# Kernel optimization log

Measured on AMD Instinct MI355X. Metric: run time of the kernel, lower is better.

## Reference

```python
import jax, jax.numpy as jnp
import numpy as np
import math

STRIDE = 32
CTR_CLAMP = 32.0
SCALE_CLAMP = math.log(1000.0 / 16)  # DEFAULT_SCALE_CLAMP
CONF_THRESH = 0.05
NMS_THRESH = 0.6
TOPK = 1000
NUM_CLASSES = 80
CLASS_OFFSET = 1.0e5  # separates classes so one IoU pass == per-class NMS


def setup_inputs() -> dict:
    key = jax.random.key(0)
    k1, k2 = jax.random.split(key)
    fmp_h, fmp_w = 100, 100
    A = 5
    M = fmp_h * fmp_w * A  # 50000 candidates
    cls_pred = jax.random.normal(k1, (M, NUM_CLASSES), dtype=jnp.float32)
    reg_pred = jax.random.normal(k2, (M, 4), dtype=jnp.float32)
    anchor_size = jnp.array([[32, 32], [64, 64], [128, 128], [256, 256], [512, 512]], dtype=jnp.float32)
    return {"cls_pred": cls_pred, "reg_pred": reg_pred, "anchor_size": anchor_size,
            "fmp_h": fmp_h, "fmp_w": fmp_w}


def _generate_anchors(anchor_size, fmp_h, fmp_w):
    # anchors laid out as [H*W, A, 4] -> [M, 4], matching torch.meshgrid order
    ys, xs = jnp.meshgrid(jnp.arange(fmp_h, dtype=jnp.float32),
                          jnp.arange(fmp_w, dtype=jnp.float32), indexing="ij")
    xy = (jnp.stack([xs, ys], axis=-1).reshape(-1, 2) + 0.5) * STRIDE  # [HW, 2]
    A = anchor_size.shape[0]
    anchor_xy = jnp.repeat(xy[:, None, :], A, axis=1)                   # [HW, A, 2]
    anchor_wh = jnp.broadcast_to(anchor_size[None], (xy.shape[0], A, 2))
    return jnp.concatenate([anchor_xy, anchor_wh], axis=-1).reshape(-1, 4)  # [M, 4]


def _decode_boxes(anchors, reg):
    # anchors/reg: [K, 4] (cx, cy, w, h) / (dx, dy, dw, dh)
    ctr_off = jnp.clip(reg[:, :2] * anchors[:, 2:], -CTR_CLAMP, CTR_CLAMP)
    ctr_xy = anchors[:, :2] + ctr_off
    wh = anchors[:, 2:] * jnp.exp(jnp.minimum(reg[:, 2:], SCALE_CLAMP))
    return jnp.concatenate([ctr_xy - 0.5 * wh, ctr_xy + 0.5 * wh], axis=-1)  # x1y1x2y2


def _greedy_nms_keep(boxes, valid):
    # boxes: [K, 4] already score-sorted descending; valid: [K] bool
    x1, y1, x2, y2 = boxes[:, 0], boxes[:, 1], boxes[:, 2], boxes[:, 3]
    areas = (x2 - x1) * (y2 - y1)
    xx1 = jnp.maximum(x1[:, None], x1[None, :])
    yy1 = jnp.maximum(y1[:, None], y1[None, :])
    xx2 = jnp.minimum(x2[:, None], x2[None, :])
    yy2 = jnp.minimum(y2[:, None], y2[None, :])
    inter = jnp.maximum(1e-28, xx2 - xx1) * jnp.maximum(1e-28, yy2 - yy1)
    iou = inter / (areas[:, None] + areas[None, :] - inter + 1e-14)  # [K, K]
    idxs = jnp.arange(boxes.shape[0])

    def body(i, keep):
        suppress = keep[i] & (iou[i] > NMS_THRESH) & (idxs > i)
        return keep & ~suppress

    return jax.lax.fori_loop(0, boxes.shape[0], body, valid)


def reference(cls_pred, reg_pred, anchor_size, fmp_h, fmp_w):
    anchors = _generate_anchors(anchor_size, fmp_h, fmp_w)  # [M, 4]
    probs = jax.nn.sigmoid(cls_pred)                        # [M, C]
    scores = probs.max(axis=-1)
    labels = probs.argmax(axis=-1)
    # top-k candidates (lax.top_k returns scores sorted descending)
    scores, idx = jax.lax.top_k(scores, TOPK)
    labels = labels[idx]
    reg = reg_pred[idx]
    anc = anchors[idx]
    boxes = _decode_boxes(anc, reg)                         # [K, 4] in pixels
    valid = scores >= CONF_THRESH
    # per-class NMS via class offsets (boxes of different classes never overlap)
    boxes_off = boxes + labels.astype(boxes.dtype)[:, None] * CLASS_OFFSET
    keep = _greedy_nms_keep(boxes_off, valid)
    img_w = fmp_w * STRIDE
    img_h = fmp_h * STRIDE
    scale = jnp.array([img_w, img_h, img_w, img_h], dtype=boxes.dtype)
    nboxes = jnp.clip(boxes / scale, 0.0, 1.0)
    m = keep.astype(boxes.dtype)
    return nboxes * m[:, None], scores * m, jnp.where(keep, labels, -1), keep
```

## Files before the change

### kernel.cpp

```cpp
#include <hip/hip_runtime.h>
#include <math.h>

#define NCLS 80
#define TOPK 1000
#define NWORDS 16
#define CAND_CAP 4096

__device__ __forceinline__ float sigmoid_np(float x) {
  float e = (float)exp(-(double)x);
  return 1.0f / (1.0f + e);
}
__device__ __forceinline__ float exp_np(float x) { return (float)exp((double)x); }

__device__ __forceinline__ unsigned fkey(float s) {
  unsigned u = __float_as_uint(s);
  return ((int)u < 0) ? ~u : (u | 0x80000000u);
}

__device__ __forceinline__ void agg_add(unsigned* h, unsigned bin, bool pred) {
  unsigned long long rem = __ballot(pred);
  const int lane = threadIdx.x & 63;
  while (rem) {
    int leader = __ffsll(rem) - 1;
    unsigned lb = (unsigned)__shfl((int)bin, leader, 64);
    unsigned long long m = __ballot(pred && bin == lb);
    if (lane == leader) atomicAdd(&h[lb], (unsigned)__popcll(m));
    rem &= ~m;
  }
}

__launch_bounds__(1024)
__global__ void k_score(const float* __restrict__ cls, float* __restrict__ scores,
                        int* __restrict__ labels, unsigned* __restrict__ ghist1, int M) {
  __shared__ unsigned h1[4096];
  const int t = threadIdx.x;
  #pragma unroll
  for (int k = 0; k < 4; ++k) h1[t + 1024 * k] = 0u;
  __syncthreads();

  int gid = blockIdx.x * 1024 + t;
  int anchor = gid >> 2;
  int q = gid & 3;
  bool act = anchor < M;
  float lv[20];
  float best = -3.4e38f; int bc = 0;
  if (act) {
    const float4* row = reinterpret_cast<const float4*>(cls) + (size_t)anchor * (NCLS / 4);
    #pragma unroll
    for (int k = 0; k < 5; ++k) {
      float4 v = row[q + 4 * k];
      int cbase = (q + 4 * k) * 4;
      lv[4 * k + 0] = v.x; lv[4 * k + 1] = v.y; lv[4 * k + 2] = v.z; lv[4 * k + 3] = v.w;
      if (v.x > best) { best = v.x; bc = cbase + 0; }
      if (v.y > best) { best = v.y; bc = cbase + 1; }
      if (v.z > best) { best = v.z; bc = cbase + 2; }
      if (v.w > best) { best = v.w; bc = cbase + 3; }
    }
  } else {
    #pragma unroll
    for (int k = 0; k < 20; ++k) lv[k] = -3.4e38f;
  }
  #pragma unroll
  for (int d = 1; d < 4; d <<= 1) {
    float ob = __shfl_xor(best, d, 64);
    int oc = __shfl_xor(bc, d, 64);
    if (ob > best || (ob == best && oc < bc)) { best = ob; bc = oc; }
  }
  float s = sigmoid_np(best);
  float sp = s * (1.0f - s);
  float band = (s < 1.0f && sp > 0.0f) ? (4.8e-7f / sp) : 3.4e38f;
  float thresh = best - band;
  int cclose = 1 << 30;
  #pragma unroll
  for (int k = 0; k < 5; ++k) {
    #pragma unroll
    for (int j = 0; j < 4; ++j) {
      int c = (q + 4 * k) * 4 + j;
      if (lv[4 * k + j] >= thresh && c < cclose) cclose = c;
    }
  }
  #pragma unroll
  for (int d = 1; d < 4; d <<= 1) {
    int oc = __shfl_xor(cclose, d, 64);
    if (oc < cclose) cclose = oc;
  }
  int lab = bc;
  if (act && cclose < bc && q == 0) {
    float bp = -1.0f; int bl = 0;
    for (int c = 0; c < NCLS; ++c) {
      float p = sigmoid_np(cls[(size_t)anchor * NCLS + c]);
      if (p > bp) { bp = p; bl = c; }
    }
    lab = bl;
  }
  if (act && q == 0) {
    scores[anchor] = s;
    labels[anchor] = lab;
  }
  agg_add(h1, fkey(s) >> 20, act && q == 0);
  __syncthreads();
  #pragma unroll
  for (int k = 0; k < 4; ++k) {
    unsigned c = h1[t + 1024 * k];
    if (c) atomicAdd(&ghist1[t + 1024 * k], c);
  }
}

__launch_bounds__(1024)
__global__ void k_hist2(const unsigned* __restrict__ ghist1, const float* __restrict__ scores,
                        unsigned* __restrict__ ghist2, unsigned* __restrict__ gmeta, int M) {
  __shared__ unsigned chunks[1024];
  __shared__ int sB1; __shared__ unsigned sAb;
  const int t = threadIdx.x;
  unsigned hb0 = ghist1[4 * t], hb1 = ghist1[4 * t + 1],
           hb2 = ghist1[4 * t + 2], hb3 = ghist1[4 * t + 3];
  chunks[t] = hb0 + hb1 + hb2 + hb3;
  __syncthreads();
  for (int d = 1; d < 1024; d <<= 1) {
    unsigned v = chunks[t] + ((t + d < 1024) ? chunks[t + d] : 0u);
    __syncthreads();
    chunks[t] = v;
    __syncthreads();
  }
  {
    unsigned ssc = chunks[t];
    unsigned ssn = (t + 1 < 1024) ? chunks[t + 1] : 0u;
    if (ssc >= (unsigned)TOPK && ssn < (unsigned)TOPK) {
      unsigned hb[4] = {hb0, hb1, hb2, hb3};
      unsigned run = ssn;
      for (int b = 3; b >= 0; --b) {
        run += hb[b];
        if (run >= (unsigned)TOPK) { sB1 = 4 * t + b; sAb = run - hb[b]; break; }
      }
    }
  }
  __syncthreads();
  const unsigned B1 = (unsigned)sB1;
  if (blockIdx.x == 0 && t == 0) { gmeta[0] = B1; gmeta[1] = sAb; }

  int base = (blockIdx.x * 1024 + t) * 4;
  if (base + 3 < M) {
    float4 v = *reinterpret_cast<const float4*>(scores + base);
    unsigned k0 = fkey(v.x), k1 = fkey(v.y), k2 = fkey(v.z), k3 = fkey(v.w);
    if ((k0 >> 20) == B1) atomicAdd(&ghist2[(k0 >> 8) & 0xFFFu], 1u);
    if ((k1 >> 20) == B1) atomicAdd(&ghist2[(k1 >> 8) & 0xFFFu], 1u);
    if ((k2 >> 20) == B1) atomicAdd(&ghist2[(k2 >> 8) & 0xFFFu], 1u);
    if ((k3 >> 20) == B1) atomicAdd(&ghist2[(k3 >> 8) & 0xFFFu], 1u);
  } else {
    for (int j = base; j < M; ++j) {
      unsigned k0 = fkey(scores[j]);
      if ((k0 >> 20) == B1) atomicAdd(&ghist2[(k0 >> 8) & 0xFFFu], 1u);
    }
  }
}

__launch_bounds__(1024)
__global__ void k_compact(const unsigned* __restrict__ ghist2, const unsigned* __restrict__ gmeta,
                          const float* __restrict__ scores,
                          unsigned long long* __restrict__ cand, unsigned* __restrict__ gcount,
                          int M) {
  __shared__ unsigned chunks[1024];
  __shared__ int sB2;
  __shared__ unsigned wcnt[16];
  __shared__ unsigned sbase;
  const int t = threadIdx.x;
  const unsigned B1 = gmeta[0], nAb = gmeta[1];
  unsigned hb0 = ghist2[4 * t], hb1 = ghist2[4 * t + 1],
           hb2 = ghist2[4 * t + 2], hb3 = ghist2[4 * t + 3];
  chunks[t] = hb0 + hb1 + hb2 + hb3;
  __syncthreads();
  for (int d = 1; d < 1024; d <<= 1) {
    unsigned v = chunks[t] + ((t + d < 1024) ? chunks[t + d] : 0u);
    __syncthreads();
    chunks[t] = v;
    __syncthreads();
  }
  {
    unsigned ssc = nAb + chunks[t];
    unsigned ssn = nAb + ((t + 1 < 1024) ? chunks[t + 1] : 0u);
    if (ssc >= (unsigned)TOPK && ssn < (unsigned)TOPK) {
      unsigned hb[4] = {hb0, hb1, hb2, hb3};
      unsigned run = ssn;
      for (int b = 3; b >= 0; --b) {
        run += hb[b];
        if (run >= (unsigned)TOPK) { sB2 = 4 * t + b; break; }
      }
    }
  }
  __syncthreads();
  const unsigned T = (B1 << 20) | ((unsigned)sB2 << 8);

  int base = (blockIdx.x * 1024 + t) * 4;
  unsigned keys[4]; int idxs[4]; int np = 0;
  #pragma unroll
  for (int j = 0; j < 4; ++j) {
    int i = base + j;
    if (i < M) {
      unsigned key = fkey(scores[i]);
      if (key >= T) { keys[np] = key; idxs[np] = i; ++np; }
    }
  }
  const int lane = t & 63, wid = t >> 6;
  int sc = np;
  #pragma unroll
  for (int d = 1; d < 64; d <<= 1) {
    int o = __shfl_up(sc, d, 64);
    if (lane >= d) sc += o;
  }
  if (lane == 63) wcnt[wid] = (unsigned)sc;
  __syncthreads();
  if (t == 0) {
    unsigned acc = 0;
    for (int w = 0; w < 16; ++w) { unsigned v = wcnt[w]; wcnt[w] = acc; acc += v; }
    sbase = acc ? atomicAdd(gcount, acc) : 0u;
  }
  __syncthreads();
  unsigned pos = sbase + wcnt[wid] + (unsigned)(sc - np);
  for (int j = 0; j < np; ++j) {
    if (pos < (unsigned)CAND_CAP)
      cand[pos] = ((unsigned long long)keys[j] << 32) | (unsigned)(~(unsigned)idxs[j]);
    ++pos;
  }
}

__launch_bounds__(1024)
__global__ void k_rank(const unsigned long long* __restrict__ cand, const unsigned* __restrict__ gcount,
                       const int* __restrict__ labels, const float* __restrict__ reg,
                       const float* __restrict__ asz, const int* __restrict__ pW, int A,
                       float* __restrict__ sel_score, int* __restrict__ sel_label,
                       float* __restrict__ boxes, float* __restrict__ areas,
                       float* __restrict__ obox) {
  __shared__ unsigned long long ck[CAND_CAP];
  const int t = threadIdx.x;
  unsigned n = *gcount; if (n > (unsigned)CAND_CAP) n = (unsigned)CAND_CAP;
  for (int i = t; i < CAND_CAP; i += 1024) ck[i] = (i < (int)n) ? cand[i] : 0ull;
  __syncthreads();
  for (int c = t; c < (int)n; c += 1024) {
    unsigned long long my = ck[c];
    int r = 0;
    for (int j = 0; j < (int)n; ++j) r += (ck[j] > my);
    if (r < TOPK) {
      unsigned key = (unsigned)(my >> 32);
      unsigned u = (key & 0x80000000u) ? (key ^ 0x80000000u) : ~key;
      float scv = __uint_as_float(u);
      int idx = (int)(~(unsigned)my);
      int lab = labels[idx];
      int W = *pW;
      int a = idx % A;
      int cell = idx / A;
      int x = cell % W;
      int y = cell / W;
      float aw = asz[a * 2 + 0], ah = asz[a * 2 + 1];
      float ax = ((float)x + 0.5f) * 32.0f;
      float ay = ((float)y + 0.5f) * 32.0f;
      float4 rg = *reinterpret_cast<const float4*>(reg + (size_t)idx * 4);
      float offx = fminf(fmaxf(rg.x * aw, -32.0f), 32.0f);
      float offy = fminf(fmaxf(rg.y * ah, -32.0f), 32.0f);
      float cx = ax + offx, cy = ay + offy;
      const float SC = 4.135166556742356f;
      float bw = aw * exp_np(fminf(rg.z, SC));
      float bh = ah * exp_np(fminf(rg.w, SC));
      float x1 = cx - 0.5f * bw, y1 = cy - 0.5f * bh;
      float x2 = cx + 0.5f * bw, y2 = cy + 0.5f * bh;
      float off = (float)lab * 100000.0f;
      float ox1 = x1 + off, oy1 = y1 + off, ox2 = x2 + off, oy2 = y2 + off;
      sel_score[r] = scv; sel_label[r] = lab;
      boxes[r * 4 + 0] = x1; boxes[r * 4 + 1] = y1;
      boxes[r * 4 + 2] = x2; boxes[r * 4 + 3] = y2;
      obox[0 * 1024 + r] = ox1; obox[1 * 1024 + r] = oy1;
      obox[2 * 1024 + r] = ox2; obox[3 * 1024 + r] = oy2;
      areas[r] = (ox2 - ox1) * (oy2 - oy1);
    }
  }
}

__launch_bounds__(256)
__global__ void k_mask(const float* __restrict__ obox, const float* __restrict__ areas,
                       unsigned long long* __restrict__ maskC) {
  __shared__ float so0[1024], so1[1024], so2[1024], so3[1024], sa[1024];
  const int t = threadIdx.x;
  int g = blockIdx.x * 256 + t;
  int c = g >> 10, j = g & 1023;
  for (int idx = t; idx < 1024; idx += 256) {
    so0[idx] = obox[idx];        so1[idx] = obox[1024 + idx];
    so2[idx] = obox[2048 + idx]; so3[idx] = obox[3072 + idx];
    sa[idx] = areas[idx];
  }
  __syncthreads();
  if (j >= TOPK) { maskC[c * 1024 + j] = 0ull; return; }
  float x1j = so0[j], y1j = so1[j], x2j = so2[j], y2j = so3[j];
  float aj = sa[j];
  unsigned long long bits = 0ull;
  int i0 = c * 64;
  for (int ii = 0; ii < 64; ++ii) {
    int i = i0 + ii;
    if (i < TOPK && i < j) {
      float xx1 = fmaxf(so0[i], x1j);
      float yy1 = fmaxf(so1[i], y1j);
      float xx2 = fminf(so2[i], x2j);
      float yy2 = fminf(so3[i], y2j);
      float inter = fmaxf(1e-28f, xx2 - xx1) * fmaxf(1e-28f, yy2 - yy1);
      float uni = sa[i] + aj - inter + 1e-14f;
      float iou = inter / uni;
      if (iou > 0.6f) bits |= (1ull << ii);
    }
  }
  maskC[c * 1024 + j] = bits;
}

__launch_bounds__(512, 1)
__global__ void k_nms(const unsigned long long* __restrict__ maskC,
                      const float* __restrict__ sel_score, const int* __restrict__ sel_label,
                      const float* __restrict__ boxes,
                      const int* __restrict__ pW, const int* __restrict__ pH,
                      float* __restrict__ out) {
  __shared__ unsigned long long sm[16 * 16 * 64];
  __shared__ float ssc[1024];
  __shared__ unsigned long long kwS[16];
  const int tid = threadIdx.x;
  const int wv = tid >> 6, lane = tid & 63;

  {
    int pair = 0;
    #pragma unroll
    for (int f = 0; f < 16; ++f) {
      #pragma unroll
      for (int g = f; g < 16; ++g) {
        if ((pair & 7) == wv)
          sm[(f * 16 + g) * 64 + lane] = maskC[f * 1024 + g * 64 + lane];
        ++pair;
      }
    }
  }
  for (int i = tid; i < 1024; i += 512)
    ssc[i] = (i < TOPK) ? sel_score[i] : 0.0f;
  __syncthreads();

  if (tid < 64) {
    unsigned long long supp[16];
    #pragma unroll
    for (int f = 0; f < 16; ++f) supp[f] = 0ull;
    #pragma unroll
    for (int f = 0; f < 16; ++f) {
      unsigned long long ct = sm[(f * 16 + f) * 64 + lane];
      unsigned long long w[16];
      #pragma unroll
      for (int g = f + 1; g < 16; ++g) w[g] = sm[(f * 16 + g) * 64 + lane];
      int r = f * 64 + lane;
      unsigned long long valid = __ballot((r < TOPK) && (ssc[r] >= 0.05f));
      unsigned long long sup_any = __ballot(ct != 0ull);
      unsigned long long avail = valid & ~supp[f];
      unsigned long long kwf = 0ull;
      while (avail) {
        unsigned long long fs = avail & sup_any;
        if (!fs) { kwf |= avail; break; }
        int i = __ffsll((long long)fs) - 1;
        unsigned long long below = (1ull << i) - 1ull;
        kwf |= avail & below;
        kwf |= (1ull << i);
        unsigned long long vict = __ballot(((ct >> i) & 1ull) != 0ull);
        avail &= ~vict;
        avail &= ~(below | (1ull << i));
      }
      if (lane == 0) kwS[f] = kwf;
      #pragma unroll
      for (int g = f + 1; g < 16; ++g)
        supp[g] |= __ballot((w[g] & kwf) != 0ull);
    }
  }
  __syncthreads();

  float sw = (float)(*pW * 32);
  float sh = (float)(*pH * 32);
  const float4* b4 = reinterpret_cast<const float4*>(boxes);
  for (int r = tid; r < TOPK; r += 512) {
    bool kp = (kwS[r >> 6] >> (r & 63)) & 1ull;
    float m = kp ? 1.0f : 0.0f;
    float4 b = b4[r];
    float b0 = fminf(fmaxf(b.x / sw, 0.0f), 1.0f) * m;
    float b1 = fminf(fmaxf(b.y / sh, 0.0f), 1.0f) * m;
    float b2 = fminf(fmaxf(b.z / sw, 0.0f), 1.0f) * m;
    float b3 = fminf(fmaxf(b.w / sh, 0.0f), 1.0f) * m;
    out[r * 4 + 0] = b0; out[r * 4 + 1] = b1;
    out[r * 4 + 2] = b2; out[r * 4 + 3] = b3;
    out[TOPK * 4 + r] = ssc[r] * m;
    out[TOPK * 5 + r] = kp ? (float)sel_label[r] : -1.0f;
    out[TOPK * 6 + r] = m;
  }
}

extern "C" void kernel_launch(void* const* d_in, const int* in_sizes, int n_in,
                              void* d_out, int out_size, void* d_ws, size_t ws_size,
                              hipStream_t stream) {
  const float* cls = (const float*)d_in[0];
  const float* reg = (const float*)d_in[1];
  const float* asz = (const float*)d_in[2];
  const int* pH = (const int*)d_in[3];
  const int* pW = (const int*)d_in[4];
  int M = in_sizes[0] / NCLS;
  int A = in_sizes[2] / 2;

  char* ws = (char*)d_ws;
  size_t off = 0;
  auto alloc = [&](size_t bytes) { size_t o = off; off = (off + bytes + 255) & ~(size_t)255; return o; };
  size_t o_h1    = alloc(4096 * sizeof(unsigned));
  size_t o_h2    = alloc(4096 * sizeof(unsigned));
  size_t o_misc  = alloc(256);
  size_t zero_end = off;
  size_t o_cand  = alloc((size_t)CAND_CAP * sizeof(unsigned long long));
  size_t o_sc    = alloc((size_t)M * sizeof(float));
  size_t o_lb    = alloc((size_t)M * sizeof(int));
  size_t o_ssc   = alloc(1024 * sizeof(float));
  size_t o_slb   = alloc(1024 * sizeof(int));
  size_t o_box   = alloc((size_t)TOPK * 4 * sizeof(float));
  size_t o_area  = alloc(1024 * sizeof(float));
  size_t o_obox  = alloc(4 * 1024 * sizeof(float));
  size_t o_mask  = alloc((size_t)NWORDS * 1024 * sizeof(unsigned long long));
  (void)ws_size; (void)out_size; (void)n_in;

  hipMemsetAsync(ws, 0, zero_end, stream);

  int nblk_score = (M * 4 + 1023) / 1024;
  k_score<<<nblk_score, 1024, 0, stream>>>(
      cls, (float*)(ws + o_sc), (int*)(ws + o_lb), (unsigned*)(ws + o_h1), M);

  int nblk_scan = ((M + 3) / 4 + 1023) / 1024;
  k_hist2<<<nblk_scan, 1024, 0, stream>>>(
      (const unsigned*)(ws + o_h1), (const float*)(ws + o_sc),
      (unsigned*)(ws + o_h2), (unsigned*)(ws + o_misc + 8), M);
  k_compact<<<nblk_scan, 1024, 0, stream>>>(
      (const unsigned*)(ws + o_h2), (const unsigned*)(ws + o_misc + 8),
      (const float*)(ws + o_sc),
      (unsigned long long*)(ws + o_cand), (unsigned*)(ws + o_misc), M);
  k_rank<<<1, 1024, 0, stream>>>(
      (const unsigned long long*)(ws + o_cand), (const unsigned*)(ws + o_misc),
      (const int*)(ws + o_lb), reg, asz, pW, A,
      (float*)(ws + o_ssc), (int*)(ws + o_slb),
      (float*)(ws + o_box), (float*)(ws + o_area), (float*)(ws + o_obox));
  k_mask<<<(NWORDS * 1024) / 256, 256, 0, stream>>>(
      (const float*)(ws + o_obox), (const float*)(ws + o_area),
      (unsigned long long*)(ws + o_mask));
  k_nms<<<1, 512, 0, stream>>>(
      (const unsigned long long*)(ws + o_mask),
      (const float*)(ws + o_ssc), (const int*)(ws + o_slb),
      (const float*)(ws + o_box), pW, pH, (float*)d_out);
}
```

Measured before the change: 76.77 us.

## Fuse all pipeline stages into one cooperative persistent kernel with grid syncs

Replaces the memset and six separate kernel launches with a single cooperative kernel of 256 blocks by 512 threads. Stages are separated by grid.sync instead of kernel boundaries, and shared memory is reused through a union. The NMS mask tiles are also stored compactly in upper-triangular form. The aim is to remove per-launch overhead and the idle gaps between small serial stages, in exchange for grid-wide barrier cost and lower parallelism in the wide scoring stage.

```diff
diff --git a/kernel.cpp b/kernel.cpp
--- a/kernel.cpp
+++ b/kernel.cpp
@@ -1,10 +1,15 @@
 #include <hip/hip_runtime.h>
+#include <hip/hip_cooperative_groups.h>
 #include <math.h>
+
+namespace cg = cooperative_groups;
 
 #define NCLS 80
 #define TOPK 1000
-#define NWORDS 16
 #define CAND_CAP 4096
+#define NBLK 256
+#define NTHR 512
+#define TRI_IDX(f, g) ((f) * 16 - ((f) * ((f) - 1)) / 2 + ((g) - (f)))
 
 __device__ __forceinline__ float sigmoid_np(float x) {
   float e = (float)exp(-(double)x);
@@ -29,363 +34,340 @@
   }
 }
 
-__launch_bounds__(1024)
-__global__ void k_score(const float* __restrict__ cls, float* __restrict__ scores,
-                        int* __restrict__ labels, unsigned* __restrict__ ghist1, int M) {
-  __shared__ unsigned h1[4096];
-  const int t = threadIdx.x;
+union BigLds {
+  unsigned h1[4096];
+  unsigned chunks[512];
+  unsigned long long ck[CAND_CAP];
+  struct { float so0[1024], so1[1024], so2[1024], so3[1024], sa[1024]; } d;
+  struct { unsigned long long sm[8704]; float ssc[1024];
+           int pf[136], pg[136]; unsigned long long kwS[16]; } e;
+};
+
+__global__ void __launch_bounds__(512) k_all(
+    const float* __restrict__ cls, const float* __restrict__ reg,
+    const float* __restrict__ asz, const int* __restrict__ pW,
+    const int* __restrict__ pH,
+    float* __restrict__ scores, int* __restrict__ labels,
+    unsigned* __restrict__ ghist1, unsigned* __restrict__ ghist2,
+    unsigned* __restrict__ gcount, unsigned long long* __restrict__ cand,
+    float* __restrict__ sel_score, int* __restrict__ sel_label,
+    float* __restrict__ boxesO, float* __restrict__ areas,
+    float* __restrict__ obox, unsigned long long* __restrict__ maskC,
+    float* __restrict__ out, int M, int A) {
+  cg::grid_group grid = cg::this_grid();
+  const int tid = threadIdx.x;
+  const int b = blockIdx.x;
+  const int tg = b * NTHR + tid;
+  const int lane = tid & 63;
+  __shared__ BigLds L;
+  __shared__ int sB1; __shared__ unsigned sAb; __shared__ int sB2;
+
+  if (tg < 4096) ghist1[tg] = 0u;
+  else if (tg < 8192) ghist2[tg - 4096] = 0u;
+  else if (tg == 8192) *gcount = 0u;
+  grid.sync();
+
   #pragma unroll
-  for (int k = 0; k < 4; ++k) h1[t + 1024 * k] = 0u;
-  __syncthreads();
-
-  int gid = blockIdx.x * 1024 + t;
-  int anchor = gid >> 2;
-  int q = gid & 3;
-  bool act = anchor < M;
-  float lv[20];
-  float best = -3.4e38f; int bc = 0;
-  if (act) {
-    const float4* row = reinterpret_cast<const float4*>(cls) + (size_t)anchor * (NCLS / 4);
-    #pragma unroll
-    for (int k = 0; k < 5; ++k) {
-      float4 v = row[q + 4 * k];
-      int cbase = (q + 4 * k) * 4;
-      lv[4 * k + 0] = v.x; lv[4 * k + 1] = v.y; lv[4 * k + 2] = v.z; lv[4 * k + 3] = v.w;
-      if (v.x > best) { best = v.x; bc = cbase + 0; }
-      if (v.y > best) { best = v.y; bc = cbase + 1; }
-      if (v.z > best) { best = v.z; bc = cbase + 2; }
-      if (v.w > best) { best = v.w; bc = cbase + 3; }
-    }
-  } else {
-    #pragma unroll
-    for (int k = 0; k < 20; ++k) lv[k] = -3.4e38f;
-  }
-  #pragma unroll
-  for (int d = 1; d < 4; d <<= 1) {
-    float ob = __shfl_xor(best, d, 64);
-    int oc = __shfl_xor(bc, d, 64);
-    if (ob > best || (ob == best && oc < bc)) { best = ob; bc = oc; }
-  }
-  float s = sigmoid_np(best);
-  float sp = s * (1.0f - s);
-  float band = (s < 1.0f && sp > 0.0f) ? (4.8e-7f / sp) : 3.4e38f;
-  float thresh = best - band;
-  int cclose = 1 << 30;
-  #pragma unroll
-  for (int k = 0; k < 5; ++k) {
-    #pragma unroll
-    for (int j = 0; j < 4; ++j) {
-      int c = (q + 4 * k) * 4 + j;
-      if (lv[4 * k + j] >= thresh && c < cclose) cclose = c;
-    }
-  }
-  #pragma unroll
-  for (int d = 1; d < 4; d <<= 1) {
-    int oc = __shfl_xor(cclose, d, 64);
-    if (oc < cclose) cclose = oc;
-  }
-  int lab = bc;
-  if (act && cclose < bc && q == 0) {
-    float bp = -1.0f; int bl = 0;
-    for (int c = 0; c < NCLS; ++c) {
-      float p = sigmoid_np(cls[(size_t)anchor * NCLS + c]);
-      if (p > bp) { bp = p; bl = c; }
-    }
-    lab = bl;
-  }
-  if (act && q == 0) {
-    scores[anchor] = s;
-    labels[anchor] = lab;
-  }
-  agg_add(h1, fkey(s) >> 20, act && q == 0);
+  for (int k = 0; k < 8; ++k) L.h1[tid + 512 * k] = 0u;
   __syncthreads();
   #pragma unroll
-  for (int k = 0; k < 4; ++k) {
-    unsigned c = h1[t + 1024 * k];
-    if (c) atomicAdd(&ghist1[t + 1024 * k], c);
-  }
-}
-
-__launch_bounds__(1024)
-__global__ void k_hist2(const unsigned* __restrict__ ghist1, const float* __restrict__ scores,
-                        unsigned* __restrict__ ghist2, unsigned* __restrict__ gmeta, int M) {
-  __shared__ unsigned chunks[1024];
-  __shared__ int sB1; __shared__ unsigned sAb;
-  const int t = threadIdx.x;
-  unsigned hb0 = ghist1[4 * t], hb1 = ghist1[4 * t + 1],
-           hb2 = ghist1[4 * t + 2], hb3 = ghist1[4 * t + 3];
-  chunks[t] = hb0 + hb1 + hb2 + hb3;
+  for (int k = 0; k < 2; ++k) {
+    int task = tg + k * (NBLK * NTHR);
+    int anchor = task >> 2, q = task & 3;
+    bool act = anchor < M;
+    float lv[20];
+    float best = -3.4e38f; int bc = 0;
+    if (act) {
+      const float4* row = reinterpret_cast<const float4*>(cls) + (size_t)anchor * (NCLS / 4);
+      #pragma unroll
+      for (int kk = 0; kk < 5; ++kk) {
+        float4 v = row[q + 4 * kk];
+        int cbase = (q + 4 * kk) * 4;
+        lv[4 * kk + 0] = v.x; lv[4 * kk + 1] = v.y; lv[4 * kk + 2] = v.z; lv[4 * kk + 3] = v.w;
+        if (v.x > best) { best = v.x; bc = cbase + 0; }
+        if (v.y > best) { best = v.y; bc = cbase + 1; }
+        if (v.z > best) { best = v.z; bc = cbase + 2; }
+        if (v.w > best) { best = v.w; bc = cbase + 3; }
+      }
+    } else {
+      #pragma unroll
+      for (int kk = 0; kk < 20; ++kk) lv[kk] = -3.4e38f;
+    }
+    #pragma unroll
+    for (int d = 1; d < 4; d <<= 1) {
+      float ob = __shfl_xor(best, d, 64);
+      int oc = __shfl_xor(bc, d, 64);
+      if (ob > best || (ob == best && oc < bc)) { best = ob; bc = oc; }
+    }
+    float s = sigmoid_np(best);
+    float sp = s * (1.0f - s);
+    float band = (s < 1.0f && sp > 0.0f) ? (4.8e-7f / sp) : 3.4e38f;
+    float thresh = best - band;
+    int cclose = 1 << 30;
+    #pragma unroll
+    for (int kk = 0; kk < 5; ++kk) {
+      #pragma unroll
+      for (int j = 0; j < 4; ++j) {
+        int c = (q + 4 * kk) * 4 + j;
+        if (lv[4 * kk + j] >= thresh && c < cclose) cclose = c;
+      }
+    }
+    #pragma unroll
+    for (int d = 1; d < 4; d <<= 1) {
+      int oc = __shfl_xor(cclose, d, 64);
+      if (oc < cclose) cclose = oc;
+    }
+    int lab = bc;
+    if (act && cclose < bc && q == 0) {
+      float bp = -1.0f; int bl = 0;
+      for (int c = 0; c < NCLS; ++c) {
+        float p = sigmoid_np(cls[(size_t)anchor * NCLS + c]);
+        if (p > bp) { bp = p; bl = c; }
+      }
+      lab = bl;
+    }
+    if (act && q == 0) { scores[anchor] = s; labels[anchor] = lab; }
+    agg_add(L.h1, fkey(s) >> 20, act && q == 0);
+  }
   __syncthreads();
-  for (int d = 1; d < 1024; d <<= 1) {
-    unsigned v = chunks[t] + ((t + d < 1024) ? chunks[t + d] : 0u);
-    __syncthreads();
-    chunks[t] = v;
-    __syncthreads();
-  }
+  #pragma unroll
+  for (int k = 0; k < 8; ++k) {
+    unsigned c = L.h1[tid + 512 * k];
+    if (c) atomicAdd(&ghist1[tid + 512 * k], c);
+  }
+  grid.sync();
+
   {
-    unsigned ssc = chunks[t];
-    unsigned ssn = (t + 1 < 1024) ? chunks[t + 1] : 0u;
+    unsigned hb[8];
+    #pragma unroll
+    for (int i = 0; i < 8; ++i) hb[i] = ghist1[tid * 8 + i];
+    unsigned s8 = hb[0] + hb[1] + hb[2] + hb[3] + hb[4] + hb[5] + hb[6] + hb[7];
+    L.chunks[tid] = s8;
+    __syncthreads();
+    for (int d = 1; d < 512; d <<= 1) {
+      unsigned v = L.chunks[tid] + ((tid + d < 512) ? L.chunks[tid + d] : 0u);
+      __syncthreads(); L.chunks[tid] = v; __syncthreads();
+    }
+    unsigned ssc = L.chunks[tid];
+    unsigned ssn = (tid + 1 < 512) ? L.chunks[tid + 1] : 0u;
     if (ssc >= (unsigned)TOPK && ssn < (unsigned)TOPK) {
-      unsigned hb[4] = {hb0, hb1, hb2, hb3};
       unsigned run = ssn;
-      for (int b = 3; b >= 0; --b) {
-        run += hb[b];
-        if (run >= (unsigned)TOPK) { sB1 = 4 * t + b; sAb = run - hb[b]; break; }
-      }
-    }
-  }
-  __syncthreads();
+      for (int bb = 7; bb >= 0; --bb) {
+        run += hb[bb];
+        if (run >= (unsigned)TOPK) { sB1 = tid * 8 + bb; sAb = run - hb[bb]; break; }
+      }
+    }
+    __syncthreads();
+  }
   const unsigned B1 = (unsigned)sB1;
-  if (blockIdx.x == 0 && t == 0) { gmeta[0] = B1; gmeta[1] = sAb; }
-
-  int base = (blockIdx.x * 1024 + t) * 4;
-  if (base + 3 < M) {
-    float4 v = *reinterpret_cast<const float4*>(scores + base);
+  const unsigned nAb = sAb;
+  const int M4 = M >> 2;
+  const float4* s4 = reinterpret_cast<const float4*>(scores);
+  if (tg < M4) {
+    float4 v = s4[tg];
     unsigned k0 = fkey(v.x), k1 = fkey(v.y), k2 = fkey(v.z), k3 = fkey(v.w);
     if ((k0 >> 20) == B1) atomicAdd(&ghist2[(k0 >> 8) & 0xFFFu], 1u);
     if ((k1 >> 20) == B1) atomicAdd(&ghist2[(k1 >> 8) & 0xFFFu], 1u);
     if ((k2 >> 20) == B1) atomicAdd(&ghist2[(k2 >> 8) & 0xFFFu], 1u);
     if ((k3 >> 20) == B1) atomicAdd(&ghist2[(k3 >> 8) & 0xFFFu], 1u);
-  } else {
-    for (int j = base; j < M; ++j) {
-      unsigned k0 = fkey(scores[j]);
-      if ((k0 >> 20) == B1) atomicAdd(&ghist2[(k0 >> 8) & 0xFFFu], 1u);
-    }
-  }
-}
-
-__launch_bounds__(1024)
-__global__ void k_compact(const unsigned* __restrict__ ghist2, const unsigned* __restrict__ gmeta,
-                          const float* __restrict__ scores,
-                          unsigned long long* __restrict__ cand, unsigned* __restrict__ gcount,
-                          int M) {
-  __shared__ unsigned chunks[1024];
-  __shared__ int sB2;
-  __shared__ unsigned wcnt[16];
-  __shared__ unsigned sbase;
-  const int t = threadIdx.x;
-  const unsigned B1 = gmeta[0], nAb = gmeta[1];
-  unsigned hb0 = ghist2[4 * t], hb1 = ghist2[4 * t + 1],
-           hb2 = ghist2[4 * t + 2], hb3 = ghist2[4 * t + 3];
-  chunks[t] = hb0 + hb1 + hb2 + hb3;
-  __syncthreads();
-  for (int d = 1; d < 1024; d <<= 1) {
-    unsigned v = chunks[t] + ((t + d < 1024) ? chunks[t + d] : 0u);
-    __syncthreads();
-    chunks[t] = v;
-    __syncthreads();
-  }
+  }
+  grid.sync();
+
   {
-    unsigned ssc = nAb + chunks[t];
-    unsigned ssn = nAb + ((t + 1 < 1024) ? chunks[t + 1] : 0u);
+    unsigned hb[8];
+    #pragma unroll
+    for (int i = 0; i < 8; ++i) hb[i] = ghist2[tid * 8 + i];
+    unsigned s8 = hb[0] + hb[1] + hb[2] + hb[3] + hb[4] + hb[5] + hb[6] + hb[7];
+    L.chunks[tid] = s8;
+    __syncthreads();
+    for (int d = 1; d < 512; d <<= 1) {
+      unsigned v = L.chunks[tid] + ((tid + d < 512) ? L.chunks[tid + d] : 0u);
+      __syncthreads(); L.chunks[tid] = v; __syncthreads();
+    }
+    unsigned ssc = nAb + L.chunks[tid];
+    unsigned ssn = nAb + ((tid + 1 < 512) ? L.chunks[tid + 1] : 0u);
     if (ssc >= (unsigned)TOPK && ssn < (unsigned)TOPK) {
-      unsigned hb[4] = {hb0, hb1, hb2, hb3};
       unsigned run = ssn;
-      for (int b = 3; b >= 0; --b) {
-        run += hb[b];
-        if (run >= (unsigned)TOPK) { sB2 = 4 * t + b; break; }
-      }
-    }
-  }
-  __syncthreads();
+      for (int bb = 7; bb >= 0; --bb) {
+        run += hb[bb];
+        if (run >= (unsigned)TOPK) { sB2 = tid * 8 + bb; break; }
+      }
+    }
+    __syncthreads();
+  }
   const unsigned T = (B1 << 20) | ((unsigned)sB2 << 8);
-
-  int base = (blockIdx.x * 1024 + t) * 4;
-  unsigned keys[4]; int idxs[4]; int np = 0;
-  #pragma unroll
-  for (int j = 0; j < 4; ++j) {
-    int i = base + j;
-    if (i < M) {
-      unsigned key = fkey(scores[i]);
-      if (key >= T) { keys[np] = key; idxs[np] = i; ++np; }
-    }
-  }
-  const int lane = t & 63, wid = t >> 6;
-  int sc = np;
-  #pragma unroll
-  for (int d = 1; d < 64; d <<= 1) {
-    int o = __shfl_up(sc, d, 64);
-    if (lane >= d) sc += o;
-  }
-  if (lane == 63) wcnt[wid] = (unsigned)sc;
-  __syncthreads();
-  if (t == 0) {
-    unsigned acc = 0;
-    for (int w = 0; w < 16; ++w) { unsigned v = wcnt[w]; wcnt[w] = acc; acc += v; }
-    sbase = acc ? atomicAdd(gcount, acc) : 0u;
-  }
-  __syncthreads();
-  unsigned pos = sbase + wcnt[wid] + (unsigned)(sc - np);
-  for (int j = 0; j < np; ++j) {
-    if (pos < (unsigned)CAND_CAP)
-      cand[pos] = ((unsigned long long)keys[j] << 32) | (unsigned)(~(unsigned)idxs[j]);
-    ++pos;
-  }
-}
-
-__launch_bounds__(1024)
-__global__ void k_rank(const unsigned long long* __restrict__ cand, const unsigned* __restrict__ gcount,
-                       const int* __restrict__ labels, const float* __restrict__ reg,
-                       const float* __restrict__ asz, const int* __restrict__ pW, int A,
-                       float* __restrict__ sel_score, int* __restrict__ sel_label,
-                       float* __restrict__ boxes, float* __restrict__ areas,
-                       float* __restrict__ obox) {
-  __shared__ unsigned long long ck[CAND_CAP];
-  const int t = threadIdx.x;
-  unsigned n = *gcount; if (n > (unsigned)CAND_CAP) n = (unsigned)CAND_CAP;
-  for (int i = t; i < CAND_CAP; i += 1024) ck[i] = (i < (int)n) ? cand[i] : 0ull;
-  __syncthreads();
-  for (int c = t; c < (int)n; c += 1024) {
-    unsigned long long my = ck[c];
-    int r = 0;
-    for (int j = 0; j < (int)n; ++j) r += (ck[j] > my);
-    if (r < TOPK) {
-      unsigned key = (unsigned)(my >> 32);
-      unsigned u = (key & 0x80000000u) ? (key ^ 0x80000000u) : ~key;
-      float scv = __uint_as_float(u);
-      int idx = (int)(~(unsigned)my);
-      int lab = labels[idx];
-      int W = *pW;
-      int a = idx % A;
-      int cell = idx / A;
-      int x = cell % W;
-      int y = cell / W;
-      float aw = asz[a * 2 + 0], ah = asz[a * 2 + 1];
-      float ax = ((float)x + 0.5f) * 32.0f;
-      float ay = ((float)y + 0.5f) * 32.0f;
-      float4 rg = *reinterpret_cast<const float4*>(reg + (size_t)idx * 4);
-      float offx = fminf(fmaxf(rg.x * aw, -32.0f), 32.0f);
-      float offy = fminf(fmaxf(rg.y * ah, -32.0f), 32.0f);
-      float cx = ax + offx, cy = ay + offy;
-      const float SC = 4.135166556742356f;
-      float bw = aw * exp_np(fminf(rg.z, SC));
-      float bh = ah * exp_np(fminf(rg.w, SC));
-      float x1 = cx - 0.5f * bw, y1 = cy - 0.5f * bh;
-      float x2 = cx + 0.5f * bw, y2 = cy + 0.5f * bh;
-      float off = (float)lab * 100000.0f;
-      float ox1 = x1 + off, oy1 = y1 + off, ox2 = x2 + off, oy2 = y2 + off;
-      sel_score[r] = scv; sel_label[r] = lab;
-      boxes[r * 4 + 0] = x1; boxes[r * 4 + 1] = y1;
-      boxes[r * 4 + 2] = x2; boxes[r * 4 + 3] = y2;
-      obox[0 * 1024 + r] = ox1; obox[1 * 1024 + r] = oy1;
-      obox[2 * 1024 + r] = ox2; obox[3 * 1024 + r] = oy2;
-      areas[r] = (ox2 - ox1) * (oy2 - oy1);
-    }
-  }
-}
-
-__launch_bounds__(256)
-__global__ void k_mask(const float* __restrict__ obox, const float* __restrict__ areas,
-                       unsigned long long* __restrict__ maskC) {
-  __shared__ float so0[1024], so1[1024], so2[1024], so3[1024], sa[1024];
-  const int t = threadIdx.x;
-  int g = blockIdx.x * 256 + t;
-  int c = g >> 10, j = g & 1023;
-  for (int idx = t; idx < 1024; idx += 256) {
-    so0[idx] = obox[idx];        so1[idx] = obox[1024 + idx];
-    so2[idx] = obox[2048 + idx]; so3[idx] = obox[3072 + idx];
-    sa[idx] = areas[idx];
-  }
-  __syncthreads();
-  if (j >= TOPK) { maskC[c * 1024 + j] = 0ull; return; }
-  float x1j = so0[j], y1j = so1[j], x2j = so2[j], y2j = so3[j];
-  float aj = sa[j];
-  unsigned long long bits = 0ull;
-  int i0 = c * 64;
-  for (int ii = 0; ii < 64; ++ii) {
-    int i = i0 + ii;
-    if (i < TOPK && i < j) {
-      float xx1 = fmaxf(so0[i], x1j);
-      float yy1 = fmaxf(so1[i], y1j);
-      float xx2 = fminf(so2[i], x2j);
-      float yy2 = fminf(so3[i], y2j);
-      float inter = fmaxf(1e-28f, xx2 - xx1) * fmaxf(1e-28f, yy2 - yy1);
-      float uni = sa[i] + aj - inter + 1e-14f;
-      float iou = inter / uni;
-      if (iou > 0.6f) bits |= (1ull << ii);
-    }
-  }
-  maskC[c * 1024 + j] = bits;
-}
-
-__launch_bounds__(512, 1)
-__global__ void k_nms(const unsigned long long* __restrict__ maskC,
-                      const float* __restrict__ sel_score, const int* __restrict__ sel_label,
-                      const float* __restrict__ boxes,
-                      const int* __restrict__ pW, const int* __restrict__ pH,
-                      float* __restrict__ out) {
-  __shared__ unsigned long long sm[16 * 16 * 64];
-  __shared__ float ssc[1024];
-  __shared__ unsigned long long kwS[16];
-  const int tid = threadIdx.x;
-  const int wv = tid >> 6, lane = tid & 63;
-
   {
-    int pair = 0;
-    #pragma unroll
-    for (int f = 0; f < 16; ++f) {
-      #pragma unroll
-      for (int g = f; g < 16; ++g) {
-        if ((pair & 7) == wv)
-          sm[(f * 16 + g) * 64 + lane] = maskC[f * 1024 + g * 64 + lane];
-        ++pair;
-      }
-    }
-  }
-  for (int i = tid; i < 1024; i += 512)
-    ssc[i] = (i < TOPK) ? sel_score[i] : 0.0f;
-  __syncthreads();
-
-  if (tid < 64) {
-    unsigned long long supp[16];
-    #pragma unroll
-    for (int f = 0; f < 16; ++f) supp[f] = 0ull;
-    #pragma unroll
-    for (int f = 0; f < 16; ++f) {
-      unsigned long long ct = sm[(f * 16 + f) * 64 + lane];
-      unsigned long long w[16];
-      #pragma unroll
-      for (int g = f + 1; g < 16; ++g) w[g] = sm[(f * 16 + g) * 64 + lane];
-      int r = f * 64 + lane;
-      unsigned long long valid = __ballot((r < TOPK) && (ssc[r] >= 0.05f));
-      unsigned long long sup_any = __ballot(ct != 0ull);
-      unsigned long long avail = valid & ~supp[f];
-      unsigned long long kwf = 0ull;
-      while (avail) {
-        unsigned long long fs = avail & sup_any;
-        if (!fs) { kwf |= avail; break; }
-        int i = __ffsll((long long)fs) - 1;
-        unsigned long long below = (1ull << i) - 1ull;
-        kwf |= avail & below;
-        kwf |= (1ull << i);
-        unsigned long long vict = __ballot(((ct >> i) & 1ull) != 0ull);
-        avail &= ~vict;
-        avail &= ~(below | (1ull << i));
-      }
-      if (lane == 0) kwS[f] = kwf;
-      #pragma unroll
-      for (int g = f + 1; g < 16; ++g)
-        supp[g] |= __ballot((w[g] & kwf) != 0ull);
-    }
-  }
-  __syncthreads();
-
-  float sw = (float)(*pW * 32);
-  float sh = (float)(*pH * 32);
-  const float4* b4 = reinterpret_cast<const float4*>(boxes);
-  for (int r = tid; r < TOPK; r += 512) {
-    bool kp = (kwS[r >> 6] >> (r & 63)) & 1ull;
-    float m = kp ? 1.0f : 0.0f;
-    float4 b = b4[r];
-    float b0 = fminf(fmaxf(b.x / sw, 0.0f), 1.0f) * m;
-    float b1 = fminf(fmaxf(b.y / sh, 0.0f), 1.0f) * m;
-    float b2 = fminf(fmaxf(b.z / sw, 0.0f), 1.0f) * m;
-    float b3 = fminf(fmaxf(b.w / sh, 0.0f), 1.0f) * m;
-    out[r * 4 + 0] = b0; out[r * 4 + 1] = b1;
-    out[r * 4 + 2] = b2; out[r * 4 + 3] = b3;
-    out[TOPK * 4 + r] = ssc[r] * m;
-    out[TOPK * 5 + r] = kp ? (float)sel_label[r] : -1.0f;
-    out[TOPK * 6 + r] = m;
+    unsigned keys[4]; int idxs[4]; int np = 0;
+    if (tg < M4) {
+      float4 v = s4[tg];
+      unsigned kk[4] = {fkey(v.x), fkey(v.y), fkey(v.z), fkey(v.w)};
+      #pragma unroll
+      for (int j = 0; j < 4; ++j)
+        if (kk[j] >= T) { keys[np] = kk[j]; idxs[np] = tg * 4 + j; ++np; }
+    }
+    int sc = np;
+    #pragma unroll
+    for (int d = 1; d < 64; d <<= 1) {
+      int o = __shfl_up(sc, d, 64);
+      if (lane >= d) sc += o;
+    }
+    unsigned base = 0;
+    int wtot = __shfl(sc, 63, 64);
+    if (lane == 63 && sc > 0) base = atomicAdd(gcount, (unsigned)sc);
+    base = (unsigned)__shfl((int)base, 63, 64);
+    (void)wtot;
+    unsigned pos = base + (unsigned)(sc - np);
+    for (int j = 0; j < np; ++j) {
+      if (pos < (unsigned)CAND_CAP)
+        cand[pos] = ((unsigned long long)keys[j] << 32) | (unsigned)(~(unsigned)idxs[j]);
+      ++pos;
+    }
+  }
+  grid.sync();
+
+  {
+    unsigned n = *gcount; if (n > (unsigned)CAND_CAP) n = (unsigned)CAND_CAP;
+    for (int i = tid; i < (int)n; i += NTHR) L.ck[i] = cand[i];
+    __syncthreads();
+    int spb = ((int)n + NBLK - 1) / NBLK;
+    int c = b * spb + tid;
+    if (tid < spb && c < (int)n) {
+      unsigned long long my = L.ck[c];
+      int r = 0;
+      for (int j = 0; j < (int)n; ++j) r += (L.ck[j] > my);
+      if (r < TOPK) {
+        unsigned key = (unsigned)(my >> 32);
+        unsigned u = (key & 0x80000000u) ? (key ^ 0x80000000u) : ~key;
+        float scv = __uint_as_float(u);
+        int idx = (int)(~(unsigned)my);
+        int lab = labels[idx];
+        int W = *pW;
+        int a = idx % A;
+        int cell = idx / A;
+        int x = cell % W;
+        int y = cell / W;
+        float aw = asz[a * 2 + 0], ah = asz[a * 2 + 1];
+        float ax = ((float)x + 0.5f) * 32.0f;
+        float ay = ((float)y + 0.5f) * 32.0f;
+        float4 rg = *reinterpret_cast<const float4*>(reg + (size_t)idx * 4);
+        float offx = fminf(fmaxf(rg.x * aw, -32.0f), 32.0f);
+        float offy = fminf(fmaxf(rg.y * ah, -32.0f), 32.0f);
+        float cx = ax + offx, cy = ay + offy;
+        const float SC = 4.135166556742356f;
+        float bw = aw * exp_np(fminf(rg.z, SC));
+        float bh = ah * exp_np(fminf(rg.w, SC));
+        float x1 = cx - 0.5f * bw, y1 = cy - 0.5f * bh;
+        float x2 = cx + 0.5f * bw, y2 = cy + 0.5f * bh;
+        float off = (float)lab * 100000.0f;
+        float ox1 = x1 + off, oy1 = y1 + off, ox2 = x2 + off, oy2 = y2 + off;
+        sel_score[r] = scv; sel_label[r] = lab;
+        boxesO[r * 4 + 0] = x1; boxesO[r * 4 + 1] = y1;
+        boxesO[r * 4 + 2] = x2; boxesO[r * 4 + 3] = y2;
+        obox[0 * 1024 + r] = ox1; obox[1 * 1024 + r] = oy1;
+        obox[2 * 1024 + r] = ox2; obox[3 * 1024 + r] = oy2;
+        areas[r] = (ox2 - ox1) * (oy2 - oy1);
+      }
+    }
+  }
+  grid.sync();
+
+  if (b < 32) {
+    for (int i = tid; i < 1024; i += NTHR) {
+      L.d.so0[i] = obox[i];        L.d.so1[i] = obox[1024 + i];
+      L.d.so2[i] = obox[2048 + i]; L.d.so3[i] = obox[3072 + i];
+      L.d.sa[i] = areas[i];
+    }
+    __syncthreads();
+    int t5 = b * NTHR + tid;
+    int c5 = t5 >> 10, j = t5 & 1023;
+    unsigned long long bits = 0ull;
+    if (j < TOPK) {
+      float x1j = L.d.so0[j], y1j = L.d.so1[j], x2j = L.d.so2[j], y2j = L.d.so3[j];
+      float aj = L.d.sa[j];
+      int i0 = c5 * 64;
+      for (int ii = 0; ii < 64; ++ii) {
+        int i = i0 + ii;
+        if (i < TOPK && i < j) {
+          float xx1 = fmaxf(L.d.so0[i], x1j);
+          float yy1 = fmaxf(L.d.so1[i], y1j);
+          float xx2 = fminf(L.d.so2[i], x2j);
+          float yy2 = fminf(L.d.so3[i], y2j);
+          float inter = fmaxf(1e-28f, xx2 - xx1) * fmaxf(1e-28f, yy2 - yy1);
+          float uni = L.d.sa[i] + aj - inter + 1e-14f;
+          float iou = inter / uni;
+          if (iou > 0.6f) bits |= (1ull << ii);
+        }
+      }
+    }
+    maskC[c5 * 1024 + j] = bits;
+  }
+  grid.sync();
+
+  if (b == 0) {
+    if (tid < 136) {
+      int p = tid, f = 0;
+      while (p >= 16 - f) { p -= 16 - f; ++f; }
+      L.e.pf[tid] = f; L.e.pg[tid] = f + p;
+    }
+    for (int i = tid; i < 1024; i += NTHR)
+      L.e.ssc[i] = (i < TOPK) ? sel_score[i] : 0.0f;
+    __syncthreads();
+    #pragma unroll
+    for (int k = 0; k < 17; ++k) {
+      int i = tid + k * NTHR;
+      int p = i >> 6, l = i & 63;
+      L.e.sm[i] = maskC[L.e.pf[p] * 1024 + L.e.pg[p] * 64 + l];
+    }
+    __syncthreads();
+
+    if (tid < 64) {
+      unsigned long long supp[16];
+      #pragma unroll
+      for (int f = 0; f < 16; ++f) supp[f] = 0ull;
+      #pragma unroll
+      for (int f = 0; f < 16; ++f) {
+        unsigned long long ct = L.e.sm[TRI_IDX(f, f) * 64 + lane];
+        int r = f * 64 + lane;
+        unsigned long long valid = __ballot((r < TOPK) && (L.e.ssc[r] >= 0.05f));
+        unsigned long long sup_any = __ballot(ct != 0ull);
+        unsigned long long avail = valid & ~supp[f];
+        unsigned long long kwf = 0ull;
+        while (avail) {
+          unsigned long long fs = avail & sup_any;
+          if (!fs) { kwf |= avail; break; }
+          int i = __ffsll((long long)fs) - 1;
+          unsigned long long below = (1ull << i) - 1ull;
+          kwf |= avail & below;
+          kwf |= (1ull << i);
+          unsigned long long vict = __ballot(((ct >> i) & 1ull) != 0ull);
+          avail &= ~vict;
+          avail &= ~(below | (1ull << i));
+        }
+        if (lane == 0) L.e.kwS[f] = kwf;
+        #pragma unroll
+        for (int g = f + 1; g < 16; ++g)
+          supp[g] |= __ballot((L.e.sm[TRI_IDX(f, g) * 64 + lane] & kwf) != 0ull);
+      }
+    }
+    __syncthreads();
+
+    float sw = (float)(*pW * 32);
+    float sh = (float)(*pH * 32);
+    const float4* b4 = reinterpret_cast<const float4*>(boxesO);
+    for (int r = tid; r < TOPK; r += NTHR) {
+      bool kp = (L.e.kwS[r >> 6] >> (r & 63)) & 1ull;
+      float m = kp ? 1.0f : 0.0f;
+      float4 bx = b4[r];
+      float b0 = fminf(fmaxf(bx.x / sw, 0.0f), 1.0f) * m;
+      float b1 = fminf(fmaxf(bx.y / sh, 0.0f), 1.0f) * m;
+      float b2 = fminf(fmaxf(bx.z / sw, 0.0f), 1.0f) * m;
+      float b3 = fminf(fmaxf(bx.w / sh, 0.0f), 1.0f) * m;
+      out[r * 4 + 0] = b0; out[r * 4 + 1] = b1;
+      out[r * 4 + 2] = b2; out[r * 4 + 3] = b3;
+      out[TOPK * 4 + r] = L.e.ssc[r] * m;
+      out[TOPK * 5 + r] = kp ? (float)sel_label[r] : -1.0f;
+      out[TOPK * 6 + r] = m;
+    }
   }
 }
 
@@ -403,45 +385,41 @@
   char* ws = (char*)d_ws;
   size_t off = 0;
   auto alloc = [&](size_t bytes) { size_t o = off; off = (off + bytes + 255) & ~(size_t)255; return o; };
-  size_t o_h1    = alloc(4096 * sizeof(unsigned));
-  size_t o_h2    = alloc(4096 * sizeof(unsigned));
-  size_t o_misc  = alloc(256);
-  size_t zero_end = off;
-  size_t o_cand  = alloc((size_t)CAND_CAP * sizeof(unsigned long long));
-  size_t o_sc    = alloc((size_t)M * sizeof(float));
-  size_t o_lb    = alloc((size_t)M * sizeof(int));
-  size_t o_ssc   = alloc(1024 * sizeof(float));
-  size_t o_slb   = alloc(1024 * sizeof(int));
-  size_t o_box   = alloc((size_t)TOPK * 4 * sizeof(float));
-  size_t o_area  = alloc(1024 * sizeof(float));
-  size_t o_obox  = alloc(4 * 1024 * sizeof(float));
-  size_t o_mask  = alloc((size_t)NWORDS * 1024 * sizeof(unsigned long long));
+  size_t o_h1   = alloc(4096 * sizeof(unsigned));
+  size_t o_h2   = alloc(4096 * sizeof(unsigned));
+  size_t o_cnt  = alloc(256);
+  size_t o_cand = alloc((size_t)CAND_CAP * sizeof(unsigned long long));
+  size_t o_sc   = alloc((size_t)M * sizeof(float));
+  size_t o_lb   = alloc((size_t)M * sizeof(int));
+  size_t o_ssc  = alloc(1024 * sizeof(float));
+  size_t o_slb  = alloc(1024 * sizeof(int));
+  size_t o_box  = alloc((size_t)TOPK * 4 * sizeof(float));
+  size_t o_area = alloc(1024 * sizeof(float));
+  size_t o_obox = alloc(4 * 1024 * sizeof(float));
+  size_t o_mask = alloc((size_t)16 * 1024 * sizeof(unsigned long long));
   (void)ws_size; (void)out_size; (void)n_in;
 
-  hipMemsetAsync(ws, 0, zero_end, stream);
-
-  int nblk_score = (M * 4 + 1023) / 1024;
-  k_score<<<nblk_score, 1024, 0, stream>>>(
-      cls, (float*)(ws + o_sc), (int*)(ws + o_lb), (unsigned*)(ws + o_h1), M);
-
-  int nblk_scan = ((M + 3) / 4 + 1023) / 1024;
-  k_hist2<<<nblk_scan, 1024, 0, stream>>>(
-      (const unsigned*)(ws + o_h1), (const float*)(ws + o_sc),
-      (unsigned*)(ws + o_h2), (unsigned*)(ws + o_misc + 8), M);
-  k_compact<<<nblk_scan, 1024, 0, stream>>>(
-      (const unsigned*)(ws + o_h2), (const unsigned*)(ws + o_misc + 8),
-      (const float*)(ws + o_sc),
-      (unsigned long long*)(ws + o_cand), (unsigned*)(ws + o_misc), M);
-  k_rank<<<1, 1024, 0, stream>>>(
-      (const unsigned long long*)(ws + o_cand), (const unsigned*)(ws + o_misc),
-      (const int*)(ws + o_lb), reg, asz, pW, A,
-      (float*)(ws + o_ssc), (int*)(ws + o_slb),
-      (float*)(ws + o_box), (float*)(ws + o_area), (float*)(ws + o_obox));
-  k_mask<<<(NWORDS * 1024) / 256, 256, 0, stream>>>(
-      (const float*)(ws + o_obox), (const float*)(ws + o_area),
-      (unsigned long long*)(ws + o_mask));
-  k_nms<<<1, 512, 0, stream>>>(
-      (const unsigned long long*)(ws + o_mask),
-      (const float*)(ws + o_ssc), (const int*)(ws + o_slb),
-      (const float*)(ws + o_box), pW, pH, (float*)d_out);
+  float* scores = (float*)(ws + o_sc);
+  int* labels = (int*)(ws + o_lb);
+  unsigned* gh1 = (unsigned*)(ws + o_h1);
+  unsigned* gh2 = (unsigned*)(ws + o_h2);
+  unsigned* gcnt = (unsigned*)(ws + o_cnt);
+  unsigned long long* cand = (unsigned long long*)(ws + o_cand);
+  float* ssc = (float*)(ws + o_ssc);
+  int* slb = (int*)(ws + o_slb);
+  float* box = (float*)(ws + o_box);
+  float* area = (float*)(ws + o_area);
+  float* obox = (float*)(ws + o_obox);
+  unsigned long long* maskC = (unsigned long long*)(ws + o_mask);
+  float* outp = (float*)d_out;
+
+  void* args[] = {
+    (void*)&cls, (void*)&reg, (void*)&asz, (void*)&pW, (void*)&pH,
+    (void*)&scores, (void*)&labels, (void*)&gh1, (void*)&gh2,
+    (void*)&gcnt, (void*)&cand, (void*)&ssc, (void*)&slb,
+    (void*)&box, (void*)&area, (void*)&obox, (void*)&maskC,
+    (void*)&outp, (void*)&M, (void*)&A
+  };
+  hipLaunchCooperativeKernel((const void*)k_all, dim3(NBLK), dim3(NTHR),
+                             args, 0, stream);
 }
```

Result: slower. 205.3 us (+167.5%).
